# Kernel tuning notes

Measured on AMD Instinct MI355X. Metric: run time of the kernel, lower is better.

Reference implementation:

```python
import jax, jax.numpy as jnp
import numpy as np
from jax import lax


def setup_inputs() -> dict:
    key = jax.random.key(0)
    ks = jax.random.split(key, 8)
    B, S, H, L = 64, 512, 768, 9
    hidden = jax.random.normal(ks[0], (B, S, H), jnp.float32)
    label = jax.random.randint(ks[1], (B, S), 0, L, dtype=jnp.int32)
    mask = jnp.ones((B, S), jnp.int32)
    W = jax.random.normal(ks[2], (H, L), jnp.float32) * 0.02
    b = jnp.zeros((L,), jnp.float32)
    start_transitions = jax.random.normal(ks[3], (L,), jnp.float32) * 0.1
    end_transitions = jax.random.normal(ks[4], (L,), jnp.float32) * 0.1
    transitions = jax.random.normal(ks[5], (L, L), jnp.float32) * 0.1
    return dict(hidden=hidden, label=label, mask=mask, W=W, b=b,
                start_transitions=start_transitions,
                end_transitions=end_transitions,
                transitions=transitions)


def reference(hidden, label, mask, W, b, start_transitions, end_transitions, transitions):
    B, S, H = hidden.shape
    L = b.shape[0]
    # output_layer: [B,S,H] @ [H,L] -> emissions, then transpose to time-major [S,B,L]
    emissions = jnp.einsum('bsh,hl->bsl', hidden, W) + b
    em = jnp.transpose(emissions, (1, 0, 2))        # [S, B, L]
    tags = label.T                                   # [S, B]
    m = mask.T.astype(jnp.float32)                   # [S, B]

    def gather_tag(em_t, tag_t):
        # em_t [B,L], tag_t [B] -> [B]
        return jnp.take_along_axis(em_t, tag_t[:, None], axis=1)[:, 0]

    # ---- numerator: score of the gold path ----
    score0 = start_transitions[tags[0]] + gather_tag(em[0], tags[0])
    def num_step(carry, x):
        score, prev = carry
        em_t, tag_t, m_t = x
        s = transitions[prev, tag_t] + gather_tag(em_t, tag_t)
        score = score + s * m_t
        prev = jnp.where(m_t > 0, tag_t, prev)
        return (score, prev), None
    (score, last_gold), _ = lax.scan(num_step, (score0, tags[0]), (em[1:], tags[1:], m[1:]))
    score = score + end_transitions[last_gold]

    # ---- denominator: forward algorithm (logsumexp DP) ----
    alpha0 = start_transitions[None, :] + em[0]      # [B, L]
    def fwd_step(alpha, x):
        em_t, m_t = x
        nxt = jax.nn.logsumexp(alpha[:, :, None] + transitions[None, :, :] + em_t[:, None, :], axis=1)
        alpha = jnp.where(m_t[:, None] > 0, nxt, alpha)
        return alpha, None
    alphaT, _ = lax.scan(fwd_step, alpha0, (em[1:], m[1:]))
    logZ = jax.nn.logsumexp(alphaT + end_transitions[None, :], axis=1)

    llh = jnp.sum(score - logZ)                      # reduction='sum'
    loss = -llh / B

    # ---- Viterbi decode (decode() is called without mask -> full length) ----
    v0 = start_transitions[None, :] + em[0]
    def vit_step(v, em_t):
        scores = v[:, :, None] + transitions[None, :, :] + em_t[:, None, :]  # [B, L, L]
        return jnp.max(scores, axis=1), jnp.argmax(scores, axis=1)
    vT, hist = lax.scan(vit_step, v0, em[1:])        # hist [S-1, B, L]
    last_tag = jnp.argmax(vT + end_transitions[None, :], axis=1)  # [B]
    def back_step(tag, bp_t):
        prev = jnp.take_along_axis(bp_t, tag[:, None], axis=1)[:, 0]
        return prev, prev
    _, prevs = lax.scan(back_step, last_tag, hist, reverse=True)  # [S-1, B]
    path = jnp.concatenate([prevs, last_tag[None, :]], axis=0).T  # [B, S]

    # ---- accuracy bookkeeping (label > 0 mask) ----
    label_flat = label.reshape(-1)
    label_mask = (label_flat > 0).astype(jnp.int32)
    predict = path.reshape(-1).astype(jnp.int32) * label_mask
    correct = jnp.sum((predict == label_flat).astype(jnp.float32))
    return loss, correct, predict, label_flat
```

## Files before the change

### kernel.cpp

```cpp
#include <hip/hip_runtime.h>
#include <hip/hip_bf16.h>

#define NB 64
#define NS 512
#define NH 768
#define NL 9
#define NROWS (NB*NS)
#define EMN (NROWS*NL)

#define VST  4617
#define BPST 4616

__device__ __forceinline__ float readlane_f(float v, int l) {
    return __int_as_float(__builtin_amdgcn_readlane(__float_as_int(v), l));
}
__device__ __forceinline__ unsigned long long readlane_u64(unsigned long long v, int l) {
    unsigned int lo = (unsigned int)__builtin_amdgcn_readlane((int)(unsigned int)(v & 0xffffffffULL), l);
    unsigned int hi = (unsigned int)__builtin_amdgcn_readlane((int)(unsigned int)(v >> 32), l);
    return ((unsigned long long)hi << 32) | (unsigned long long)lo;
}
template <int CTRL>
__device__ __forceinline__ float dpp_add(float x) {
    int t = __builtin_amdgcn_update_dpp(0, __float_as_int(x), CTRL, 0xf, 0xf, false);
    return x + __int_as_float(t);
}
__device__ __forceinline__ float wave_sum_to63(float x) {
    x = dpp_add<0x111>(x);
    x = dpp_add<0x112>(x);
    x = dpp_add<0x114>(x);
    x = dpp_add<0x118>(x);
    x = dpp_add<0x142>(x);
    x = dpp_add<0x143>(x);
    return x;
}
template <int I>
__device__ __forceinline__ float rowbc(float x) {
    return __int_as_float(__builtin_amdgcn_ds_swizzle(__float_as_int(x), (I << 5) | 0x10));
}

__global__ __launch_bounds__(256) void k_gemm(const float* __restrict__ hidden,
                                              const float* __restrict__ W,
                                              const float* __restrict__ bias,
                                              float* __restrict__ em,
                                              float* __restrict__ out) {
    __shared__ float s_part[4][4][NL];
    int tid = threadIdx.x;
    int lane = tid & 63;
    int w = tid >> 6;
    int bx = blockIdx.x;
    if (bx == 0 && tid == 0) { out[0] = 0.f; out[1] = 0.f; }

    int kbase = 192 * w + lane;
    float Wv[3][NL];
#pragma unroll
    for (int c = 0; c < 3; c++) {
        const float* wp = W + (size_t)(kbase + 64 * c) * NL;
#pragma unroll
        for (int j = 0; j < NL; j++) Wv[c][j] = wp[j];
    }

#pragma unroll
    for (int r = 0; r < 4; r++) {
        int row = 4 * bx + r;
        const float* hp = hidden + (size_t)row * NH + kbase;
        float h0 = hp[0], h1 = hp[64], h2 = hp[128];
        float acc[NL];
#pragma unroll
        for (int j = 0; j < NL; j++) {
            acc[j] = fmaf(h0, Wv[0][j], fmaf(h1, Wv[1][j], h2 * Wv[2][j]));
        }
#pragma unroll
        for (int j = 0; j < NL; j++) acc[j] = wave_sum_to63(acc[j]);
        if (lane == 63) {
#pragma unroll
            for (int j = 0; j < NL; j++) s_part[w][r][j] = acc[j];
        }
    }
    __syncthreads();
    if (tid < 36) {
        int r = tid / NL, j = tid % NL;
        float v = (s_part[0][r][j] + s_part[1][r][j]) +
                  (s_part[2][r][j] + s_part[3][r][j]) + bias[j];
        em[(size_t)(4 * bx + r) * NL + j] = v;
    }
}

__global__ __launch_bounds__(256) void k_dp(const float* __restrict__ em,
                                            const int* __restrict__ label,
                                            const int* __restrict__ mask,
                                            const float* __restrict__ startT,
                                            const float* __restrict__ endT,
                                            const float* __restrict__ trans,
                                            float* __restrict__ out) {
    __shared__ float s_T[NL * NL];
    __shared__ int s_mki[4][NS];
    __shared__ float s_v[4 * VST];
    __shared__ unsigned char s_bp[4 * BPST];
    __shared__ unsigned char s_path[4 * NS];

    int bx = blockIdx.x;
    int tid = threadIdx.x;
    int lane = tid & 63;
    bool isfwd = bx < 16;
    int b0 = (isfwd ? bx : (bx - 16)) * 4;

    if (tid < NL * NL) s_T[tid] = trans[tid];
    if (isfwd) {
        for (int q = tid; q < 4 * NS / 4; q += 256)
            ((int4*)s_mki)[q] = ((const int4*)(mask + b0 * NS))[q];
    }
    __syncthreads();

    if (isfwd) {
        if (tid < 64) {
            int bb = lane >> 4;
            int jcol = lane & 15;
            int jcol9 = jcol < NL ? jcol : NL - 1;
            const float* gp = em + (size_t)(b0 + bb) * (NS * NL) + jcol9;
            float Mc0 = __expf(s_T[0 * NL + jcol9]);
            float Mc1 = __expf(s_T[1 * NL + jcol9]);
            float Mc2 = __expf(s_T[2 * NL + jcol9]);
            float Mc3 = __expf(s_T[3 * NL + jcol9]);
            float Mc4 = __expf(s_T[4 * NL + jcol9]);
            float Mc5 = __expf(s_T[5 * NL + jcol9]);
            float Mc6 = __expf(s_T[6 * NL + jcol9]);
            float Mc7 = __expf(s_T[7 * NL + jcol9]);
            float Mc8 = __expf(s_T[8 * NL + jcol9]);
            float a = __expf(startT[jcol9] + gp[0]);
            int eacc = 0;

#define FBODY(EC_, KC_) do { \
    float _w0=rowbc<0>(a),_w1=rowbc<1>(a),_w2=rowbc<2>(a),_w3=rowbc<3>(a),_w4=rowbc<4>(a), \
          _w5=rowbc<5>(a),_w6=rowbc<6>(a),_w7=rowbc<7>(a),_w8=rowbc<8>(a); \
    float _p0=_w0*Mc0,_p1=_w1*Mc1,_p2=_w2*Mc2,_p3=_w3*Mc3,_p4=_w4*Mc4, \
          _p5=_w5*Mc5,_p6=_w6*Mc6,_p7=_w7*Mc7,_p8=_w8*Mc8; \
    float _s=(((_p0+_p1)+(_p2+_p3))+((_p4+_p5)+(_p6+_p7)))+_p8; \
    float _an=(EC_)*_s; \
    a = ((KC_) > 0) ? _an : a; \
} while (0)

#define FREN() do { \
    float _c0=rowbc<0>(a),_c1=rowbc<1>(a),_c2=rowbc<2>(a),_c3=rowbc<3>(a),_c4=rowbc<4>(a), \
          _c5=rowbc<5>(a),_c6=rowbc<6>(a),_c7=rowbc<7>(a),_c8=rowbc<8>(a); \
    float _cc=(((_c0+_c1)+(_c2+_c3))+((_c4+_c5)+(_c6+_c7)))+_c8; \
    int _ex=((__float_as_int(_cc)>>23)&255)-127; \
    a=ldexpf(a,-_ex); eacc+=_ex; \
} while (0)

            float e8[8]; int k8[8];
#pragma unroll
            for (int p = 0; p < 8; p++) {
                e8[p] = __expf(gp[(1 + p) * NL]);
                k8[p] = s_mki[bb][1 + p];
            }
            for (int t0 = 1; t0 <= NS - 15; t0 += 8) {
#pragma unroll
                for (int p = 0; p < 8; p++) {
                    int t = t0 + p;
                    float ec = e8[p]; int kc = k8[p];
                    int tn = t + 8; tn = tn > NS - 1 ? NS - 1 : tn;
                    e8[p] = __expf(gp[tn * NL]);
                    k8[p] = s_mki[bb][tn];
                    FBODY(ec, kc);
                    if (p == 7) FREN();
                }
            }
#pragma unroll
            for (int p = 0; p < 7; p++) FBODY(e8[p], k8[p]);
#undef FBODY
#undef FREN
            float z = a * __expf(endT[jcol9]);
            float c0 = rowbc<0>(z), c1 = rowbc<1>(z), c2 = rowbc<2>(z);
            float c3 = rowbc<3>(z), c4 = rowbc<4>(z), c5 = rowbc<5>(z);
            float c6 = rowbc<6>(z), c7 = rowbc<7>(z), c8 = rowbc<8>(z);
            float c = (((c0 + c1) + (c2 + c3)) + ((c4 + c5) + (c6 + c7))) + c8;
            if (jcol == 0) {
                float lz = (float)eacc * 0.6931471805599453f + __logf(c);
                atomicAdd(out, lz * (1.0f / (float)NB));
            }
        } else if (tid < 128) {
            int g = lane >> 4;
            int ll = lane & 15;
            int b = b0 + g;
            const int* lb = label + b * NS;
            const float* ge = em + (size_t)b * NS * NL;
            int h = 0, sl = 0;
            for (int cch = 0; cch < 4; cch++) {
                int la8[8]; int mk8[8];
#pragma unroll
                for (int r = 0; r < 8; r++) {
                    int t = ll * 32 + cch * 8 + r;
                    la8[r] = lb[t];
                    int m = s_mki[g][t];
                    if (t == 0) m = 1;
                    mk8[r] = m;
                }
#pragma unroll
                for (int r = 0; r < 8; r++) if (mk8[r] > 0) { h = 1; sl = la8[r]; }
            }
#pragma unroll
            for (int d = 1; d < 16; d <<= 1) {
                int ho = __shfl_up(h, d, 16);
                int so = __shfl_up(sl, d, 16);
                if (!h) { h = ho; sl = so; }
            }
            int lg = __shfl(sl, 15, 16);
            int incoming = __shfl_up(sl, 1, 16);
            int labz = lb[0];
            int prevr = (ll == 0) ? labz : incoming;
            float sc = 0.f;
            for (int cch = 0; cch < 4; cch++) {
                int la8[8]; int mk8[8]; float ev8[8];
#pragma unroll
                for (int r = 0; r < 8; r++) {
                    int t = ll * 32 + cch * 8 + r;
                    la8[r] = lb[t];
                    int m = s_mki[g][t];
                    if (t == 0) m = 1;
                    mk8[r] = m;
                }
#pragma unroll
                for (int r = 0; r < 8; r++) {
                    int t = ll * 32 + cch * 8 + r;
                    ev8[r] = ge[t * NL + la8[r]];
                }
#pragma unroll
                for (int r = 0; r < 8; r++) {
                    int t = ll * 32 + cch * 8 + r;
                    if (t > 0) {
                        float s = s_T[prevr * NL + la8[r]] + ev8[r];
                        sc += s * (float)mk8[r];
                    }
                    if (mk8[r] > 0) prevr = la8[r];
                }
            }
            if (ll == 0) sc += startT[labz] + ge[labz] + endT[lg];
#pragma unroll
            for (int d = 1; d < 16; d <<= 1) sc += __shfl_xor(sc, d, 16);
            if (ll == 0) atomicAdd(out, -sc * (1.0f / (float)NB));
        }
    } else {
        if (tid < 64) {
            int bb = lane >> 4;
            int jcol = lane & 15;
            int jcol9 = jcol < NL ? jcol : NL - 1;
            const float* gv = em + (size_t)(b0 + bb) * (NS * NL) + jcol9;
            float Tc0 = s_T[0 * NL + jcol9];
            float Tc1 = s_T[1 * NL + jcol9];
            float Tc2 = s_T[2 * NL + jcol9];
            float Tc3 = s_T[3 * NL + jcol9];
            float Tc4 = s_T[4 * NL + jcol9];
            float Tc5 = s_T[5 * NL + jcol9];
            float Tc6 = s_T[6 * NL + jcol9];
            float Tc7 = s_T[7 * NL + jcol9];
            float Tc8 = s_T[8 * NL + jcol9];
            float v = startT[jcol9] + gv[0];
            int svbase = bb * VST + jcol;
            s_v[svbase] = v;

#define VBODY(EC_, T_) do { \
    float _w0=rowbc<0>(v),_w1=rowbc<1>(v),_w2=rowbc<2>(v),_w3=rowbc<3>(v),_w4=rowbc<4>(v), \
          _w5=rowbc<5>(v),_w6=rowbc<6>(v),_w7=rowbc<7>(v),_w8=rowbc<8>(v); \
    float _m0=_w0+Tc0,_m1=_w1+Tc1,_m2=_w2+Tc2,_m3=_w3+Tc3,_m4=_w4+Tc4, \
          _m5=_w5+Tc5,_m6=_w6+Tc6,_m7=_w7+Tc7,_m8=_w8+Tc8; \
    float _Ma=fmaxf(fmaxf(_m0,_m1),_m2); \
    float _Mb=fmaxf(fmaxf(_m3,_m4),_m5); \
    float _Mc=fmaxf(fmaxf(_m6,_m7),_m8); \
    v = fmaxf(fmaxf(_Ma,_Mb),_Mc) + (EC_); \
    s_v[svbase + (T_) * NL] = v; \
} while (0)

            float e8[8];
#pragma unroll
            for (int p = 0; p < 8; p++) e8[p] = gv[(1 + p) * NL];
            for (int t0 = 1; t0 <= NS - 15; t0 += 8) {
#pragma unroll
                for (int p = 0; p < 8; p++) {
                    int t = t0 + p;
                    float ec = e8[p];
                    int tn = t + 8; tn = tn > NS - 1 ? NS - 1 : tn;
                    e8[p] = gv[tn * NL];
                    VBODY(ec, t);
                }
            }
#pragma unroll
            for (int p = 0; p < 7; p++) VBODY(e8[p], 505 + p);
#undef VBODY
        }
        __syncthreads();
        for (int it = 0; it < 8; it++) {
            int item = tid + it * 256;
            int bb = item >> 9;
            int t = item & (NS - 1);
            if (t > 0) {
                const float* vpp = s_v + bb * VST + (t - 1) * NL;
                const float* ge = em + (size_t)(b0 + bb) * (NS * NL) + t * NL;
                float vp[NL], emt[NL];
#pragma unroll
                for (int i = 0; i < NL; i++) vp[i] = vpp[i];
#pragma unroll
                for (int j = 0; j < NL; j++) emt[j] = ge[j];
#pragma unroll
                for (int j = 0; j < NL; j++) {
                    float e = emt[j];
                    float val[NL];
#pragma unroll
                    for (int i = 0; i < NL; i++) val[i] = (vp[i] + s_T[i * NL + j]) + e;
                    bool c01 = val[0] >= val[1]; float m01 = c01 ? val[0] : val[1]; int i01 = c01 ? 0 : 1;
                    bool c23 = val[2] >= val[3]; float m23 = c23 ? val[2] : val[3]; int i23 = c23 ? 2 : 3;
                    bool c45 = val[4] >= val[5]; float m45 = c45 ? val[4] : val[5]; int i45 = c45 ? 4 : 5;
                    bool c67 = val[6] >= val[7]; float m67 = c67 ? val[6] : val[7]; int i67 = c67 ? 6 : 7;
                    bool ca = m01 >= m23; float ma = ca ? m01 : m23; int ia = ca ? i01 : i23;
                    bool cb = m45 >= m67; float mb = cb ? m45 : m67; int ib = cb ? i45 : i67;
                    bool cc = ma >= mb;  float mc = cc ? ma : mb;  int ic = cc ? ia : ib;
                    bool cd = mc >= val[8]; int bi = cd ? ic : 8;
                    s_bp[bb * BPST + t * NL + j] = (unsigned char)bi;
                }
            }
        }
        __syncthreads();
        {
            int w = tid >> 6;
            const float* sv = s_v + w * VST;
            const unsigned char* bpp = s_bp + w * BPST;
            unsigned char* pth = s_path + w * NS;
            float bb2 = sv[(NS - 1) * NL + 0] + endT[0]; int lt = 0;
#pragma unroll
            for (int jj = 1; jj < NL; jj++) {
                float fj = sv[(NS - 1) * NL + jj] + endT[jj];
                if (fj > bb2) { bb2 = fj; lt = jj; }
            }
            unsigned long long G[8];
#pragma unroll
            for (int r = 0; r < 8; r++) {
                int t0 = (lane * 8 + r) * NL;
                unsigned long long g = 0;
                if (lane == 0 && r == 0) {
                    g = 0x876543210ULL;
                } else {
#pragma unroll
                    for (int x = 0; x < NL; x++) g |= (unsigned long long)bpp[t0 + x] << (4 * x);
                }
                G[r] = g;
            }
            unsigned long long A = 0x876543210ULL;
#pragma unroll
            for (int r = 7; r >= 0; r--) {
                unsigned long long An = 0;
#pragma unroll
                for (int x = 0; x < NL; x++) {
                    int ax = (int)((A >> (4 * x)) & 15ULL);
                    int gvv = (int)((G[r] >> (4 * ax)) & 15ULL);
                    An |= (unsigned long long)gvv << (4 * x);
                }
                A = An;
            }
            int e = 0; int cur = lt;
            for (int llv = 63; llv >= 0; --llv) {
                if (lane == llv) e = cur;
                unsigned long long Al = readlane_u64(A, llv);
                cur = (int)((Al >> (4 * cur)) & 15ULL);
            }
            unsigned long long pw = 0; int c2 = e;
#pragma unroll
            for (int r = 7; r >= 0; r--) {
                pw |= (unsigned long long)c2 << (8 * r);
                c2 = (int)((G[r] >> (4 * c2)) & 15ULL);
            }
            *(unsigned long long*)(pth + lane * 8) = pw;
        }
        __syncthreads();
        float cnt = 0.f;
#pragma unroll
        for (int q = 0; q < 8; q++) {
            int item = tid + q * 256;
            int bb = item >> 9;
            int t = item & (NS - 1);
            int b = b0 + bb;
            int idx = b * NS + t;
            int lab = label[idx];
            int p = (int)s_path[bb * NS + t];
            int pred = (lab > 0) ? p : 0;
            out[2 + idx] = (float)pred;
            out[2 + NROWS + idx] = (float)lab;
            cnt += (pred == lab) ? 1.f : 0.f;
        }
#pragma unroll
        for (int d = 1; d < 64; d <<= 1) cnt += __shfl_xor(cnt, d);
        if ((tid & 63) == 0) atomicAdd(out + 1, cnt);
    }
}

extern "C" void kernel_launch(void* const* d_in, const int* in_sizes, int n_in,
                              void* d_out, int out_size, void* d_ws, size_t ws_size,
                              hipStream_t stream) {
    const float* hidden = (const float*)d_in[0];
    const int*   label  = (const int*)d_in[1];
    const int*   mask   = (const int*)d_in[2];
    const float* W      = (const float*)d_in[3];
    const float* bias   = (const float*)d_in[4];
    const float* startT = (const float*)d_in[5];
    const float* endT   = (const float*)d_in[6];
    const float* trans  = (const float*)d_in[7];
    float* out = (float*)d_out;

    float* em = (float*)d_ws;

    k_gemm<<<8192, 256, 0, stream>>>(hidden, W, bias, em, out);
    k_dp<<<32, 256, 0, stream>>>(em, label, mask, startT, endT, trans, out);
}
```

Measured before the change: 210.9 us.

## Remap CRF DP to quad-lane DPP exchange and persist GEMM blocks

The forward and Viterbi recurrences now give each batch row 4 lanes, each owning up to 3 tag columns. The previous row-wide ds_swizzle broadcasts (9 LDS-path ops per step) are replaced by quad_perm DPP moves, aiming to shorten the serial per-timestep latency chain. Each lane now does about three times the arithmetic per step. Separately, the GEMM kernel launches 1024 blocks that each loop over 8 row-groups, prefetching the next group's hidden values, at the cost of two block barriers per iteration.

```diff
diff --git a/kernel.cpp b/kernel.cpp
--- a/kernel.cpp
+++ b/kernel.cpp
@@ -11,9 +11,6 @@
 #define VST  4617
 #define BPST 4616
 
-__device__ __forceinline__ float readlane_f(float v, int l) {
-    return __int_as_float(__builtin_amdgcn_readlane(__float_as_int(v), l));
-}
 __device__ __forceinline__ unsigned long long readlane_u64(unsigned long long v, int l) {
     unsigned int lo = (unsigned int)__builtin_amdgcn_readlane((int)(unsigned int)(v & 0xffffffffULL), l);
     unsigned int hi = (unsigned int)__builtin_amdgcn_readlane((int)(unsigned int)(v >> 32), l);
@@ -33,9 +30,9 @@
     x = dpp_add<0x143>(x);
     return x;
 }
-template <int I>
-__device__ __forceinline__ float rowbc(float x) {
-    return __int_as_float(__builtin_amdgcn_ds_swizzle(__float_as_int(x), (I << 5) | 0x10));
+template <int CTRL>
+__device__ __forceinline__ float qperm(float x) {
+    return __int_as_float(__builtin_amdgcn_update_dpp(0, __float_as_int(x), CTRL, 0xf, 0xf, false));
 }
 
 __global__ __launch_bounds__(256) void k_gemm(const float* __restrict__ hidden,
@@ -59,29 +56,51 @@
         for (int j = 0; j < NL; j++) Wv[c][j] = wp[j];
     }
 
+    int gbase = bx * 8;
+    float ph[4][3];
 #pragma unroll
     for (int r = 0; r < 4; r++) {
-        int row = 4 * bx + r;
-        const float* hp = hidden + (size_t)row * NH + kbase;
-        float h0 = hp[0], h1 = hp[64], h2 = hp[128];
-        float acc[NL];
-#pragma unroll
-        for (int j = 0; j < NL; j++) {
-            acc[j] = fmaf(h0, Wv[0][j], fmaf(h1, Wv[1][j], h2 * Wv[2][j]));
-        }
-#pragma unroll
-        for (int j = 0; j < NL; j++) acc[j] = wave_sum_to63(acc[j]);
-        if (lane == 63) {
-#pragma unroll
-            for (int j = 0; j < NL; j++) s_part[w][r][j] = acc[j];
-        }
+        const float* hp = hidden + (size_t)(4 * gbase + r) * NH + kbase;
+        ph[r][0] = hp[0]; ph[r][1] = hp[64]; ph[r][2] = hp[128];
     }
-    __syncthreads();
-    if (tid < 36) {
-        int r = tid / NL, j = tid % NL;
-        float v = (s_part[0][r][j] + s_part[1][r][j]) +
-                  (s_part[2][r][j] + s_part[3][r][j]) + bias[j];
-        em[(size_t)(4 * bx + r) * NL + j] = v;
+#pragma unroll
+    for (int it = 0; it < 8; ++it) {
+        float ch[4][3];
+#pragma unroll
+        for (int r = 0; r < 4; r++) {
+            ch[r][0] = ph[r][0]; ch[r][1] = ph[r][1]; ch[r][2] = ph[r][2];
+        }
+        if (it < 7) {
+            int gn = gbase + it + 1;
+#pragma unroll
+            for (int r = 0; r < 4; r++) {
+                const float* hp = hidden + (size_t)(4 * gn + r) * NH + kbase;
+                ph[r][0] = hp[0]; ph[r][1] = hp[64]; ph[r][2] = hp[128];
+            }
+        }
+        int grow = gbase + it;
+#pragma unroll
+        for (int r = 0; r < 4; r++) {
+            float acc[NL];
+#pragma unroll
+            for (int j = 0; j < NL; j++) {
+                acc[j] = fmaf(ch[r][0], Wv[0][j], fmaf(ch[r][1], Wv[1][j], ch[r][2] * Wv[2][j]));
+            }
+#pragma unroll
+            for (int j = 0; j < NL; j++) acc[j] = wave_sum_to63(acc[j]);
+            if (lane == 63) {
+#pragma unroll
+                for (int j = 0; j < NL; j++) s_part[w][r][j] = acc[j];
+            }
+        }
+        __syncthreads();
+        if (tid < 36) {
+            int r = tid / NL, j = tid % NL;
+            float v = (s_part[0][r][j] + s_part[1][r][j]) +
+                      (s_part[2][r][j] + s_part[3][r][j]) + bias[j];
+            em[(size_t)(4 * grow + r) * NL + j] = v;
+        }
+        __syncthreads();
     }
 }
 
@@ -111,72 +130,99 @@
     }
     __syncthreads();
 
+#define EXCH(D0,D1,D2,D3,D4,D5,D6,D7,D8, XA_,XB_,XC_) do { \
+    D0 = qperm<0x00>(XA_); D1 = qperm<0x00>(XB_); D2 = qperm<0x00>(XC_); \
+    D3 = qperm<0x55>(XA_); D4 = qperm<0x55>(XB_); \
+    D5 = qperm<0xAA>(XA_); D6 = qperm<0xAA>(XB_); \
+    D7 = qperm<0xFF>(XA_); D8 = qperm<0xFF>(XB_); \
+} while (0)
+
     if (isfwd) {
         if (tid < 64) {
-            int bb = lane >> 4;
-            int jcol = lane & 15;
-            int jcol9 = jcol < NL ? jcol : NL - 1;
-            const float* gp = em + (size_t)(b0 + bb) * (NS * NL) + jcol9;
-            float Mc0 = __expf(s_T[0 * NL + jcol9]);
-            float Mc1 = __expf(s_T[1 * NL + jcol9]);
-            float Mc2 = __expf(s_T[2 * NL + jcol9]);
-            float Mc3 = __expf(s_T[3 * NL + jcol9]);
-            float Mc4 = __expf(s_T[4 * NL + jcol9]);
-            float Mc5 = __expf(s_T[5 * NL + jcol9]);
-            float Mc6 = __expf(s_T[6 * NL + jcol9]);
-            float Mc7 = __expf(s_T[7 * NL + jcol9]);
-            float Mc8 = __expf(s_T[8 * NL + jcol9]);
-            float a = __expf(startT[jcol9] + gp[0]);
-            int eacc = 0;
-
-#define FBODY(EC_, KC_) do { \
-    float _w0=rowbc<0>(a),_w1=rowbc<1>(a),_w2=rowbc<2>(a),_w3=rowbc<3>(a),_w4=rowbc<4>(a), \
-          _w5=rowbc<5>(a),_w6=rowbc<6>(a),_w7=rowbc<7>(a),_w8=rowbc<8>(a); \
-    float _p0=_w0*Mc0,_p1=_w1*Mc1,_p2=_w2*Mc2,_p3=_w3*Mc3,_p4=_w4*Mc4, \
-          _p5=_w5*Mc5,_p6=_w6*Mc6,_p7=_w7*Mc7,_p8=_w8*Mc8; \
-    float _s=(((_p0+_p1)+(_p2+_p3))+((_p4+_p5)+(_p6+_p7)))+_p8; \
-    float _an=(EC_)*_s; \
-    a = ((KC_) > 0) ? _an : a; \
+            if (lane < 16) {
+                int bb = lane >> 2;
+                int g = lane & 3;
+                int cA = (g == 0) ? 0 : (g == 1) ? 3 : (g == 2) ? 5 : 7;
+                int cB = (g == 0) ? 1 : (g == 1) ? 4 : (g == 2) ? 6 : 8;
+                int cC = (g == 0) ? 2 : cB;
+                const float* gpb = em + (size_t)(b0 + bb) * (NS * NL);
+                float McA[NL], McB[NL], McC[NL];
+#pragma unroll
+                for (int i = 0; i < NL; i++) {
+                    McA[i] = __expf(s_T[i * NL + cA]);
+                    McB[i] = __expf(s_T[i * NL + cB]);
+                    McC[i] = __expf(s_T[i * NL + cC]);
+                }
+                float xA = __expf(startT[cA] + gpb[cA]);
+                float xB = __expf(startT[cB] + gpb[cB]);
+                float xC = __expf(startT[cC] + gpb[cC]);
+                float a0, a1, a2, a3, a4, a5, a6, a7, a8;
+                EXCH(a0,a1,a2,a3,a4,a5,a6,a7,a8, xA, xB, xC);
+                int eacc = 0;
+
+#define FSTEP(EA_, EB_, EC_, KC_) do { \
+    float pA0=a0*McA[0],pA1=a1*McA[1],pA2=a2*McA[2],pA3=a3*McA[3],pA4=a4*McA[4], \
+          pA5=a5*McA[5],pA6=a6*McA[6],pA7=a7*McA[7],pA8=a8*McA[8]; \
+    float pB0=a0*McB[0],pB1=a1*McB[1],pB2=a2*McB[2],pB3=a3*McB[3],pB4=a4*McB[4], \
+          pB5=a5*McB[5],pB6=a6*McB[6],pB7=a7*McB[7],pB8=a8*McB[8]; \
+    float pC0=a0*McC[0],pC1=a1*McC[1],pC2=a2*McC[2],pC3=a3*McC[3],pC4=a4*McC[4], \
+          pC5=a5*McC[5],pC6=a6*McC[6],pC7=a7*McC[7],pC8=a8*McC[8]; \
+    float sA=(((pA0+pA1)+(pA2+pA3))+((pA4+pA5)+(pA6+pA7)))+pA8; \
+    float sB=(((pB0+pB1)+(pB2+pB3))+((pB4+pB5)+(pB6+pB7)))+pB8; \
+    float sC=(((pC0+pC1)+(pC2+pC3))+((pC4+pC5)+(pC6+pC7)))+pC8; \
+    float anA=(EA_)*sA, anB=(EB_)*sB, anC=(EC_)*sC; \
+    bool km = (KC_) > 0; \
+    xA = km ? anA : xA; xB = km ? anB : xB; xC = km ? anC : xC; \
+    EXCH(a0,a1,a2,a3,a4,a5,a6,a7,a8, xA, xB, xC); \
 } while (0)
 
 #define FREN() do { \
-    float _c0=rowbc<0>(a),_c1=rowbc<1>(a),_c2=rowbc<2>(a),_c3=rowbc<3>(a),_c4=rowbc<4>(a), \
-          _c5=rowbc<5>(a),_c6=rowbc<6>(a),_c7=rowbc<7>(a),_c8=rowbc<8>(a); \
-    float _cc=(((_c0+_c1)+(_c2+_c3))+((_c4+_c5)+(_c6+_c7)))+_c8; \
-    int _ex=((__float_as_int(_cc)>>23)&255)-127; \
-    a=ldexpf(a,-_ex); eacc+=_ex; \
+    float cc=(((a0+a1)+(a2+a3))+((a4+a5)+(a6+a7)))+a8; \
+    int ex=((__float_as_int(cc)>>23)&255)-127; \
+    xA=ldexpf(xA,-ex); xB=ldexpf(xB,-ex); xC=ldexpf(xC,-ex); \
+    a0=ldexpf(a0,-ex); a1=ldexpf(a1,-ex); a2=ldexpf(a2,-ex); \
+    a3=ldexpf(a3,-ex); a4=ldexpf(a4,-ex); a5=ldexpf(a5,-ex); \
+    a6=ldexpf(a6,-ex); a7=ldexpf(a7,-ex); a8=ldexpf(a8,-ex); \
+    eacc += ex; \
 } while (0)
 
-            float e8[8]; int k8[8];
-#pragma unroll
-            for (int p = 0; p < 8; p++) {
-                e8[p] = __expf(gp[(1 + p) * NL]);
-                k8[p] = s_mki[bb][1 + p];
-            }
-            for (int t0 = 1; t0 <= NS - 15; t0 += 8) {
+                float eA8[8], eB8[8], eC8[8]; int k8[8];
 #pragma unroll
                 for (int p = 0; p < 8; p++) {
-                    int t = t0 + p;
-                    float ec = e8[p]; int kc = k8[p];
-                    int tn = t + 8; tn = tn > NS - 1 ? NS - 1 : tn;
-                    e8[p] = __expf(gp[tn * NL]);
-                    k8[p] = s_mki[bb][tn];
-                    FBODY(ec, kc);
-                    if (p == 7) FREN();
-                }
-            }
-#pragma unroll
-            for (int p = 0; p < 7; p++) FBODY(e8[p], k8[p]);
-#undef FBODY
+                    int t = 1 + p;
+                    eA8[p] = __expf(gpb[t * NL + cA]);
+                    eB8[p] = __expf(gpb[t * NL + cB]);
+                    eC8[p] = __expf(gpb[t * NL + cC]);
+                    k8[p] = s_mki[bb][t];
+                }
+                for (int t0 = 1; t0 <= NS - 15; t0 += 8) {
+#pragma unroll
+                    for (int p = 0; p < 8; p++) {
+                        int t = t0 + p;
+                        float eA = eA8[p], eB = eB8[p], eC = eC8[p]; int kc = k8[p];
+                        int tn = t + 8; tn = tn > NS - 1 ? NS - 1 : tn;
+                        eA8[p] = __expf(gpb[tn * NL + cA]);
+                        eB8[p] = __expf(gpb[tn * NL + cB]);
+                        eC8[p] = __expf(gpb[tn * NL + cC]);
+                        k8[p] = s_mki[bb][tn];
+                        FSTEP(eA, eB, eC, kc);
+                        if (p == 7) FREN();
+                    }
+                }
+#pragma unroll
+                for (int p = 0; p < 7; p++) FSTEP(eA8[p], eB8[p], eC8[p], k8[p]);
+#undef FSTEP
 #undef FREN
-            float z = a * __expf(endT[jcol9]);
-            float c0 = rowbc<0>(z), c1 = rowbc<1>(z), c2 = rowbc<2>(z);
-            float c3 = rowbc<3>(z), c4 = rowbc<4>(z), c5 = rowbc<5>(z);
-            float c6 = rowbc<6>(z), c7 = rowbc<7>(z), c8 = rowbc<8>(z);
-            float c = (((c0 + c1) + (c2 + c3)) + ((c4 + c5) + (c6 + c7))) + c8;
-            if (jcol == 0) {
-                float lz = (float)eacc * 0.6931471805599453f + __logf(c);
-                atomicAdd(out, lz * (1.0f / (float)NB));
+                float z0 = a0 * __expf(endT[0]), z1 = a1 * __expf(endT[1]);
+                float z2 = a2 * __expf(endT[2]), z3 = a3 * __expf(endT[3]);
+                float z4 = a4 * __expf(endT[4]), z5 = a5 * __expf(endT[5]);
+                float z6 = a6 * __expf(endT[6]), z7 = a7 * __expf(endT[7]);
+                float z8 = a8 * __expf(endT[8]);
+                float c = (((z0 + z1) + (z2 + z3)) + ((z4 + z5) + (z6 + z7))) + z8;
+                if (g == 0) {
+                    float lz = (float)eacc * 0.6931471805599453f + __logf(c);
+                    atomicAdd(out, lz * (1.0f / (float)NB));
+                }
             }
         } else if (tid < 128) {
             int g = lane >> 4;
@@ -240,52 +286,68 @@
             if (ll == 0) atomicAdd(out, -sc * (1.0f / (float)NB));
         }
     } else {
-        if (tid < 64) {
-            int bb = lane >> 4;
-            int jcol = lane & 15;
-            int jcol9 = jcol < NL ? jcol : NL - 1;
-            const float* gv = em + (size_t)(b0 + bb) * (NS * NL) + jcol9;
-            float Tc0 = s_T[0 * NL + jcol9];
-            float Tc1 = s_T[1 * NL + jcol9];
-            float Tc2 = s_T[2 * NL + jcol9];
-            float Tc3 = s_T[3 * NL + jcol9];
-            float Tc4 = s_T[4 * NL + jcol9];
-            float Tc5 = s_T[5 * NL + jcol9];
-            float Tc6 = s_T[6 * NL + jcol9];
-            float Tc7 = s_T[7 * NL + jcol9];
-            float Tc8 = s_T[8 * NL + jcol9];
-            float v = startT[jcol9] + gv[0];
-            int svbase = bb * VST + jcol;
-            s_v[svbase] = v;
-
-#define VBODY(EC_, T_) do { \
-    float _w0=rowbc<0>(v),_w1=rowbc<1>(v),_w2=rowbc<2>(v),_w3=rowbc<3>(v),_w4=rowbc<4>(v), \
-          _w5=rowbc<5>(v),_w6=rowbc<6>(v),_w7=rowbc<7>(v),_w8=rowbc<8>(v); \
-    float _m0=_w0+Tc0,_m1=_w1+Tc1,_m2=_w2+Tc2,_m3=_w3+Tc3,_m4=_w4+Tc4, \
-          _m5=_w5+Tc5,_m6=_w6+Tc6,_m7=_w7+Tc7,_m8=_w8+Tc8; \
-    float _Ma=fmaxf(fmaxf(_m0,_m1),_m2); \
-    float _Mb=fmaxf(fmaxf(_m3,_m4),_m5); \
-    float _Mc=fmaxf(fmaxf(_m6,_m7),_m8); \
-    v = fmaxf(fmaxf(_Ma,_Mb),_Mc) + (EC_); \
-    s_v[svbase + (T_) * NL] = v; \
+        if (tid < 64 && lane < 16) {
+            int bb = lane >> 2;
+            int g = lane & 3;
+            int cA = (g == 0) ? 0 : (g == 1) ? 3 : (g == 2) ? 5 : 7;
+            int cB = (g == 0) ? 1 : (g == 1) ? 4 : (g == 2) ? 6 : 8;
+            int cC = (g == 0) ? 2 : cB;
+            const float* gpb = em + (size_t)(b0 + bb) * (NS * NL);
+            float TcA[NL], TcB[NL], TcC[NL];
+#pragma unroll
+            for (int i = 0; i < NL; i++) {
+                TcA[i] = s_T[i * NL + cA];
+                TcB[i] = s_T[i * NL + cB];
+                TcC[i] = s_T[i * NL + cC];
+            }
+            int svb = bb * VST;
+            float yA = startT[cA] + gpb[cA];
+            float yB = startT[cB] + gpb[cB];
+            float yC = startT[cC] + gpb[cC];
+            s_v[svb + cA] = yA; s_v[svb + cB] = yB; s_v[svb + cC] = yC;
+            float v0, v1, v2, v3, v4, v5, v6, v7, v8;
+            EXCH(v0,v1,v2,v3,v4,v5,v6,v7,v8, yA, yB, yC);
+
+#define VSTEP(EA_, EB_, EC_, T_) do { \
+    float mA0=v0+TcA[0],mA1=v1+TcA[1],mA2=v2+TcA[2],mA3=v3+TcA[3],mA4=v4+TcA[4], \
+          mA5=v5+TcA[5],mA6=v6+TcA[6],mA7=v7+TcA[7],mA8=v8+TcA[8]; \
+    float mB0=v0+TcB[0],mB1=v1+TcB[1],mB2=v2+TcB[2],mB3=v3+TcB[3],mB4=v4+TcB[4], \
+          mB5=v5+TcB[5],mB6=v6+TcB[6],mB7=v7+TcB[7],mB8=v8+TcB[8]; \
+    float mC0=v0+TcC[0],mC1=v1+TcC[1],mC2=v2+TcC[2],mC3=v3+TcC[3],mC4=v4+TcC[4], \
+          mC5=v5+TcC[5],mC6=v6+TcC[6],mC7=v7+TcC[7],mC8=v8+TcC[8]; \
+    float MA=fmaxf(fmaxf(fmaxf(fmaxf(mA0,mA1),mA2),fmaxf(fmaxf(mA3,mA4),mA5)),fmaxf(fmaxf(mA6,mA7),mA8)); \
+    float MB=fmaxf(fmaxf(fmaxf(fmaxf(mB0,mB1),mB2),fmaxf(fmaxf(mB3,mB4),mB5)),fmaxf(fmaxf(mB6,mB7),mB8)); \
+    float MC=fmaxf(fmaxf(fmaxf(fmaxf(mC0,mC1),mC2),fmaxf(fmaxf(mC3,mC4),mC5)),fmaxf(fmaxf(mC6,mC7),mC8)); \
+    yA = MA + (EA_); yB = MB + (EB_); yC = MC + (EC_); \
+    s_v[svb + (T_) * NL + cA] = yA; \
+    s_v[svb + (T_) * NL + cB] = yB; \
+    s_v[svb + (T_) * NL + cC] = yC; \
+    EXCH(v0,v1,v2,v3,v4,v5,v6,v7,v8, yA, yB, yC); \
 } while (0)
 
-            float e8[8];
-#pragma unroll
-            for (int p = 0; p < 8; p++) e8[p] = gv[(1 + p) * NL];
+            float eA8[8], eB8[8], eC8[8];
+#pragma unroll
+            for (int p = 0; p < 8; p++) {
+                int t = 1 + p;
+                eA8[p] = gpb[t * NL + cA];
+                eB8[p] = gpb[t * NL + cB];
+                eC8[p] = gpb[t * NL + cC];
+            }
             for (int t0 = 1; t0 <= NS - 15; t0 += 8) {
 #pragma unroll
                 for (int p = 0; p < 8; p++) {
                     int t = t0 + p;
-                    float ec = e8[p];
+                    float eA = eA8[p], eB = eB8[p], eC = eC8[p];
                     int tn = t + 8; tn = tn > NS - 1 ? NS - 1 : tn;
-                    e8[p] = gv[tn * NL];
-                    VBODY(ec, t);
-                }
-            }
-#pragma unroll
-            for (int p = 0; p < 7; p++) VBODY(e8[p], 505 + p);
-#undef VBODY
+                    eA8[p] = gpb[tn * NL + cA];
+                    eB8[p] = gpb[tn * NL + cB];
+                    eC8[p] = gpb[tn * NL + cC];
+                    VSTEP(eA, eB, eC, t);
+                }
+            }
+#pragma unroll
+            for (int p = 0; p < 7; p++) VSTEP(eA8[p], eB8[p], eC8[p], 505 + p);
+#undef VSTEP
         }
         __syncthreads();
         for (int it = 0; it < 8; it++) {
@@ -389,6 +451,7 @@
         for (int d = 1; d < 64; d <<= 1) cnt += __shfl_xor(cnt, d);
         if ((tid & 63) == 0) atomicAdd(out + 1, cnt);
     }
+#undef EXCH
 }
 
 extern "C" void kernel_launch(void* const* d_in, const int* in_sizes, int n_in,
@@ -406,6 +469,6 @@
 
     float* em = (float*)d_ws;
 
-    k_gemm<<<8192, 256, 0, stream>>>(hidden, W, bias, em, out);
+    k_gemm<<<1024, 256, 0, stream>>>(hidden, W, bias, em, out);
     k_dp<<<32, 256, 0, stream>>>(em, label, mask, startT, endT, trans, out);
 }
```

After: 273.3 us. 29.6% more time.

## Make GEMM blocks persistent with prefetch and fuse renormalization into forward step

Applied to the files above, without the earlier changes.

The emission GEMM now launches 1024 blocks, each processing 8 groups of 4 rows, and loads the next group's hidden values into registers while the current group is reduced. This is meant to hide global load latency and amortize the W register loads over more rows, at the cost of less parallelism and an extra barrier per iteration. In the forward DP, the periodic renormalization is merged into the next step so the row broadcasts are shared, shortening the serial dependency chain. The renormalization now runs at a different time step than before, which slightly changes where scaling is applied.

```diff
diff --git a/kernel.cpp b/kernel.cpp
--- a/kernel.cpp
+++ b/kernel.cpp
@@ -11,9 +11,6 @@
 #define VST  4617
 #define BPST 4616
 
-__device__ __forceinline__ float readlane_f(float v, int l) {
-    return __int_as_float(__builtin_amdgcn_readlane(__float_as_int(v), l));
-}
 __device__ __forceinline__ unsigned long long readlane_u64(unsigned long long v, int l) {
     unsigned int lo = (unsigned int)__builtin_amdgcn_readlane((int)(unsigned int)(v & 0xffffffffULL), l);
     unsigned int hi = (unsigned int)__builtin_amdgcn_readlane((int)(unsigned int)(v >> 32), l);
@@ -59,29 +56,51 @@
         for (int j = 0; j < NL; j++) Wv[c][j] = wp[j];
     }
 
+    int gbase = bx * 8;
+    float ph[4][3];
 #pragma unroll
     for (int r = 0; r < 4; r++) {
-        int row = 4 * bx + r;
-        const float* hp = hidden + (size_t)row * NH + kbase;
-        float h0 = hp[0], h1 = hp[64], h2 = hp[128];
-        float acc[NL];
-#pragma unroll
-        for (int j = 0; j < NL; j++) {
-            acc[j] = fmaf(h0, Wv[0][j], fmaf(h1, Wv[1][j], h2 * Wv[2][j]));
-        }
-#pragma unroll
-        for (int j = 0; j < NL; j++) acc[j] = wave_sum_to63(acc[j]);
-        if (lane == 63) {
-#pragma unroll
-            for (int j = 0; j < NL; j++) s_part[w][r][j] = acc[j];
-        }
+        const float* hp = hidden + (size_t)(4 * gbase + r) * NH + kbase;
+        ph[r][0] = hp[0]; ph[r][1] = hp[64]; ph[r][2] = hp[128];
     }
-    __syncthreads();
-    if (tid < 36) {
-        int r = tid / NL, j = tid % NL;
-        float v = (s_part[0][r][j] + s_part[1][r][j]) +
-                  (s_part[2][r][j] + s_part[3][r][j]) + bias[j];
-        em[(size_t)(4 * bx + r) * NL + j] = v;
+#pragma unroll
+    for (int it = 0; it < 8; ++it) {
+        float ch[4][3];
+#pragma unroll
+        for (int r = 0; r < 4; r++) {
+            ch[r][0] = ph[r][0]; ch[r][1] = ph[r][1]; ch[r][2] = ph[r][2];
+        }
+        if (it < 7) {
+            int gn = gbase + it + 1;
+#pragma unroll
+            for (int r = 0; r < 4; r++) {
+                const float* hp = hidden + (size_t)(4 * gn + r) * NH + kbase;
+                ph[r][0] = hp[0]; ph[r][1] = hp[64]; ph[r][2] = hp[128];
+            }
+        }
+        int grow = gbase + it;
+#pragma unroll
+        for (int r = 0; r < 4; r++) {
+            float acc[NL];
+#pragma unroll
+            for (int j = 0; j < NL; j++) {
+                acc[j] = fmaf(ch[r][0], Wv[0][j], fmaf(ch[r][1], Wv[1][j], ch[r][2] * Wv[2][j]));
+            }
+#pragma unroll
+            for (int j = 0; j < NL; j++) acc[j] = wave_sum_to63(acc[j]);
+            if (lane == 63) {
+#pragma unroll
+                for (int j = 0; j < NL; j++) s_part[w][r][j] = acc[j];
+            }
+        }
+        __syncthreads();
+        if (tid < 36) {
+            int r = tid / NL, j = tid % NL;
+            float v = (s_part[0][r][j] + s_part[1][r][j]) +
+                      (s_part[2][r][j] + s_part[3][r][j]) + bias[j];
+            em[(size_t)(4 * grow + r) * NL + j] = v;
+        }
+        __syncthreads();
     }
 }
 
@@ -139,12 +158,18 @@
     a = ((KC_) > 0) ? _an : a; \
 } while (0)
 
-#define FREN() do { \
-    float _c0=rowbc<0>(a),_c1=rowbc<1>(a),_c2=rowbc<2>(a),_c3=rowbc<3>(a),_c4=rowbc<4>(a), \
-          _c5=rowbc<5>(a),_c6=rowbc<6>(a),_c7=rowbc<7>(a),_c8=rowbc<8>(a); \
-    float _cc=(((_c0+_c1)+(_c2+_c3))+((_c4+_c5)+(_c6+_c7)))+_c8; \
+#define FBODY_REN(EC_, KC_) do { \
+    float _w0=rowbc<0>(a),_w1=rowbc<1>(a),_w2=rowbc<2>(a),_w3=rowbc<3>(a),_w4=rowbc<4>(a), \
+          _w5=rowbc<5>(a),_w6=rowbc<6>(a),_w7=rowbc<7>(a),_w8=rowbc<8>(a); \
+    float _cc=(((_w0+_w1)+(_w2+_w3))+((_w4+_w5)+(_w6+_w7)))+_w8; \
     int _ex=((__float_as_int(_cc)>>23)&255)-127; \
-    a=ldexpf(a,-_ex); eacc+=_ex; \
+    float _p0=_w0*Mc0,_p1=_w1*Mc1,_p2=_w2*Mc2,_p3=_w3*Mc3,_p4=_w4*Mc4, \
+          _p5=_w5*Mc5,_p6=_w6*Mc6,_p7=_w7*Mc7,_p8=_w8*Mc8; \
+    float _s=(((_p0+_p1)+(_p2+_p3))+((_p4+_p5)+(_p6+_p7)))+_p8; \
+    float _an=(EC_)*_s; \
+    a = ((KC_) > 0) ? _an : a; \
+    a = ldexpf(a, -_ex); \
+    eacc += _ex; \
 } while (0)
 
             float e8[8]; int k8[8];
@@ -161,14 +186,18 @@
                     int tn = t + 8; tn = tn > NS - 1 ? NS - 1 : tn;
                     e8[p] = __expf(gp[tn * NL]);
                     k8[p] = s_mki[bb][tn];
-                    FBODY(ec, kc);
-                    if (p == 7) FREN();
-                }
-            }
-#pragma unroll
-            for (int p = 0; p < 7; p++) FBODY(e8[p], k8[p]);
+                    if (p == 0 && t0 > 1) {
+                        FBODY_REN(ec, kc);
+                    } else {
+                        FBODY(ec, kc);
+                    }
+                }
+            }
+            FBODY_REN(e8[0], k8[0]);
+#pragma unroll
+            for (int p = 1; p < 7; p++) FBODY(e8[p], k8[p]);
 #undef FBODY
-#undef FREN
+#undef FBODY_REN
             float z = a * __expf(endT[jcol9]);
             float c0 = rowbc<0>(z), c1 = rowbc<1>(z), c2 = rowbc<2>(z);
             float c3 = rowbc<3>(z), c4 = rowbc<4>(z), c5 = rowbc<5>(z);
@@ -257,7 +286,6 @@
             float v = startT[jcol9] + gv[0];
             int svbase = bb * VST + jcol;
             s_v[svbase] = v;
-
 #define VBODY(EC_, T_) do { \
     float _w0=rowbc<0>(v),_w1=rowbc<1>(v),_w2=rowbc<2>(v),_w3=rowbc<3>(v),_w4=rowbc<4>(v), \
           _w5=rowbc<5>(v),_w6=rowbc<6>(v),_w7=rowbc<7>(v),_w8=rowbc<8>(v); \
@@ -269,7 +297,6 @@
     v = fmaxf(fmaxf(_Ma,_Mb),_Mc) + (EC_); \
     s_v[svbase + (T_) * NL] = v; \
 } while (0)
-
             float e8[8];
 #pragma unroll
             for (int p = 0; p < 8; p++) e8[p] = gv[(1 + p) * NL];
@@ -406,6 +433,6 @@
 
     float* em = (float*)d_ws;
 
-    k_gemm<<<8192, 256, 0, stream>>>(hidden, W, bias, em, out);
+    k_gemm<<<1024, 256, 0, stream>>>(hidden, W, bias, em, out);
     k_dp<<<32, 256, 0, stream>>>(em, label, mask, startT, endT, trans, out);
 }
```

Result: no change. 214.4 us (+1.6%).
